# Optimization experiments

Hardware: AMD Instinct MI355X
Metric: run time of the kernel (lower is better)

The kernel has to match this reference:

```python
import jax, jax.numpy as jnp
from jax import lax
import numpy as np

ATTN = 32  # attn_size window
PAD, SOS = 1, 2


def setup_inputs() -> dict:
    key = jax.random.key(0)
    ks = jax.random.split(key, 20)
    B, L, V, E, H = 16, 64, 32000, 512, 512
    sc = 0.02
    inp = {
        "s_tensor": jax.random.randint(ks[0], (B, L), 0, V, dtype=jnp.int32),
        "parents_tensor": jax.random.randint(ks[1], (L,), 0, L, dtype=jnp.int32),
        "emb": jax.random.normal(ks[2], (V, E), jnp.float32) * sc,
        "W_hid": jax.random.normal(ks[3], (H, H), jnp.float32) * sc,
        "b_hid": jnp.zeros((H,), jnp.float32),
        "v_w": jax.random.normal(ks[4], (H,), jnp.float32) * sc,
        "v_b": jnp.zeros((1,), jnp.float32),
        "W_ctx": jax.random.normal(ks[5], (E + H, H), jnp.float32) * sc,
        "b_ctx": jnp.zeros((H,), jnp.float32),
        "W_ih": jax.random.normal(ks[6], (H, 4 * H), jnp.float32) * sc,
        "W_hh": jax.random.normal(ks[7], (H, 4 * H), jnp.float32) * sc,
        "b_lstm": jnp.zeros((4 * H,), jnp.float32),
        "W_glob": jax.random.normal(ks[8], (3 * H, V), jnp.float32) * sc,
        "b_glob": jnp.zeros((V,), jnp.float32),
        "w_sw": jax.random.normal(ks[9], (2 * H,), jnp.float32) * sc,
        "b_sw": jnp.zeros((1,), jnp.float32),
    }
    return inp


def _decode(emb, W_hid, b_hid, v_w, v_b, W_ctx, b_ctx, W_ih, W_hh, b_lstm,
            W_glob, b_glob, w_sw, b_sw, s_tensor, parents_tensor):
    B, L = s_tensor.shape
    H = W_hid.shape[0]
    A = ATTN
    # teacher forcing: input at step t is SOS for t=0, else s_tensor[:, t-1]
    inputs = jnp.concatenate(
        [jnp.full((B, 1), SOS, s_tensor.dtype), s_tensor[:, : L - 2]], axis=1)  # [B, L-1]
    targets = s_tensor[:, 1:]  # [B, L-1]
    hs_buf0 = jnp.zeros((B, A + L, H), jnp.float32)  # past decoder hidden states (A zero-pad prefix)
    h0 = jnp.zeros((B, H), jnp.float32)
    c0 = jnp.zeros((B, H), jnp.float32)

    def step(carry, xs):
        h, c, hs_buf = carry
        tok, tgt, par, t = xs
        x = emb[tok]  # [B, E]
        # memory = last A decoder hidden states (steps t-A .. t-1)
        mem = lax.dynamic_slice(hs_buf, (0, t, 0), (B, A, H))
        # Bahdanau-style scores: v^T tanh(W_hidden(h) + mem), masked to valid window
        q = h @ W_hid + b_hid  # [B, H]
        scores = jnp.tanh(q[:, None, :] + mem) @ v_w + v_b  # [B, A]
        valid = jnp.arange(A) >= (A - t)
        scores = jnp.where(valid[None, :], scores, -1e20)
        attn = jax.nn.softmax(scores, axis=1)
        context = jnp.einsum('ba,bah->bh', attn, mem)
        hid = jax.nn.selu(jnp.concatenate([x, context], axis=1) @ W_ctx + b_ctx)
        # single-step LSTM cell (PyTorch gate order i,f,g,o)
        gates = hid @ W_ih + h @ W_hh + b_lstm
        i, f, g, o = jnp.split(gates, 4, axis=1)
        c_new = jax.nn.sigmoid(f) * c + jax.nn.sigmoid(i) * jnp.tanh(g)
        h_new = jax.nn.sigmoid(o) * jnp.tanh(c_new)
        # parent hidden state
        p = jnp.clip(par, 0, jnp.maximum(t - 1, 0))
        h_par = lax.dynamic_slice(hs_buf, (0, A + p, 0), (B, 1, H))[:, 0]
        logits = jnp.concatenate([h_new, c_new, h_par], axis=1) @ W_glob + b_glob
        logp = jax.nn.log_softmax(logits, axis=1)
        s = jax.nn.sigmoid(jnp.concatenate([h_new, c_new], axis=1) @ w_sw + b_sw)  # [B,1]
        out = s[:, None] * logp if s.ndim == 1 else s * logp  # pointer switch on global dist
        nll = -jnp.take_along_axis(out, tgt[:, None].astype(jnp.int32), axis=1)[:, 0]
        nll = jnp.where(tgt != PAD, nll, 0.0)
        pred = jnp.argmax(out, axis=1).astype(jnp.int32)
        hs_buf = lax.dynamic_update_slice(hs_buf, h_new[:, None, :], (0, A + t, 0))
        return (h_new, c_new, hs_buf), (nll, pred)

    T = L - 1
    xs = (inputs.T, targets.T, parents_tensor[:T], jnp.arange(T, dtype=jnp.int32))
    _, (nlls, preds) = lax.scan(step, (h0, c0, hs_buf0), xs)
    loss = nlls.sum() / B
    return loss, preds.T  # [B, L-1] predicted tokens


def reference(s_tensor, parents_tensor, emb, W_hid, b_hid, v_w, v_b, W_ctx, b_ctx,
              W_ih, W_hh, b_lstm, W_glob, b_glob, w_sw, b_sw):
    return _decode(emb, W_hid, b_hid, v_w, v_b, W_ctx, b_ctx, W_ih, W_hh, b_lstm,
                   W_glob, b_glob, w_sw, b_sw, s_tensor, parents_tensor)
```

## Files before the change

kernel.cpp:

```cpp
#include <hip/hip_runtime.h>
#include <math.h>

#define BB 16
#define LL 64
#define TT 63
#define HH 512
#define AA 32
#define VV 32000
#define NCHUNK 250
#define CHW 128
#define TGRP 3
#define NTG 21
#define PAD_TOK 1
#define SOS_TOK 2
#define HSROW 96
#define ZK 1536
#define FLTMAX 3.402823466e38f

__device__ __forceinline__ float sigm(float x){ return 1.0f/(1.0f + __expf(-x)); }

__global__ __launch_bounds__(256) void k_pre(const int* __restrict__ s, const float* __restrict__ emb,
                      const float* __restrict__ Wctx, const float* __restrict__ bctx,
                      float* __restrict__ xwpre)
{
    int t = blockIdx.x >> 3;
    int jc = blockIdx.x & 7;
    int tid = threadIdx.x;
    int jj = tid & 63, bq = tid >> 6;
    int j = jc*64 + jj;
    __shared__ int toks[BB];
    __shared__ float xs[BB][HH];
    if (tid < BB) {
        int b = tid;
        toks[b] = (t == 0) ? SOS_TOK : s[b*LL + (t-1)];
    }
    __syncthreads();
    for (int i = tid; i < BB*HH; i += 256) {
        int b = i >> 9, k = i & 511;
        xs[b][k] = emb[(size_t)toks[b]*HH + k];
    }
    __syncthreads();
    float acc[4];
    #pragma unroll
    for (int u = 0; u < 4; u++) acc[u] = bctx[j];
    for (int k = 0; k < HH; k += 4) {
        float w0 = Wctx[(k+0)*HH+j], w1 = Wctx[(k+1)*HH+j],
              w2 = Wctx[(k+2)*HH+j], w3 = Wctx[(k+3)*HH+j];
        #pragma unroll
        for (int u = 0; u < 4; u++) {
            int b = bq*4 + u;
            float4 hv = *reinterpret_cast<const float4*>(&xs[b][k]);
            acc[u] = fmaf(hv.x, w0, acc[u]);
            acc[u] = fmaf(hv.y, w1, acc[u]);
            acc[u] = fmaf(hv.z, w2, acc[u]);
            acc[u] = fmaf(hv.w, w3, acc[u]);
        }
    }
    #pragma unroll
    for (int u = 0; u < 4; u++) {
        int b = bq*4 + u;
        xwpre[((size_t)t*BB + b)*HH + j] = acc[u];
    }
}

__global__ __launch_bounds__(256) void k_tw(const float* __restrict__ Wg, float4* __restrict__ Wt4b)
{
    int kg = blockIdx.x / 125;
    int cb = blockIdx.x % 125;
    int col = cb*256 + threadIdx.x;
    const float* w0 = Wg + (size_t)(4*kg)*VV + col;
    float4 v;
    v.x = w0[0];
    v.y = w0[VV];
    v.z = w0[2*VV];
    v.w = w0[3*VV];
    Wt4b[(size_t)(col >> 6)*(384*64) + kg*64 + (col & 63)] = v;
}

__global__ __launch_bounds__(256) void k_twl(const float* __restrict__ W, float4* __restrict__ WT)
{
    int kg = blockIdx.x >> 3;
    int cb = blockIdx.x & 7;
    int col = cb*256 + threadIdx.x;
    const float* w0 = W + (size_t)(4*kg)*2048 + col;
    float4 v;
    v.x = w0[0];
    v.y = w0[2048];
    v.z = w0[2*2048];
    v.w = w0[3*2048];
    WT[(size_t)kg*2048 + col] = v;
}

__device__ void finish_step(int tp, int b, int tid,
                            const int* __restrict__ s,
                            const float* __restrict__ lb,
                            const float* __restrict__ pmax,
                            const float* __restrict__ spart,
                            const float* __restrict__ bsw,
                            float* __restrict__ nll, float* __restrict__ out,
                            float* cv, int* ci, double* sdd, float* extra)
{
    float v = -FLTMAX;
    if (tid < NCHUNK) v = pmax[tid*BB + b];
    cv[tid] = v; __syncthreads();
    for (int sft = 256; sft >= 1; sft >>= 1) {
        if (tid < sft) cv[tid] = fmaxf(cv[tid], cv[tid+sft]);
        __syncthreads();
    }
    float gmax = cv[0];
    __syncthreads();

    const float* Lb = lb + (size_t)b*VV;
    double sd = 0.0;
    for (int col = tid; col < VV; col += 512) {
        float d1 = Lb[col] - gmax;
        double u = (double)d1, e;
        if (u < -0.25) {
            e = exp(u);
        } else {
            e = 1.0 + u*(1.0/7.0);
            e = 1.0 + u*e*(1.0/6.0);
            e = 1.0 + u*e*(1.0/5.0);
            e = 1.0 + u*e*(1.0/4.0);
            e = 1.0 + u*e*(1.0/3.0);
            e = 1.0 + u*e*(1.0/2.0);
            e = 1.0 + u*e;
        }
        sd += e;
    }
    sdd[tid] = sd; __syncthreads();
    for (int sft = 256; sft >= 1; sft >>= 1) {
        if (tid < sft) sdd[tid] += sdd[tid+sft];
        __syncthreads();
    }
    float logS = logf((float)sdd[0]);

    float z = bsw[0];
    #pragma unroll
    for (int i2 = 0; i2 < 8; i2++) z += spart[b*8 + i2];
    float sF = 1.0f/(1.0f + expf(-z));
    __syncthreads();

    int tg = s[b*LL + tp + 1];
    float best = -FLTMAX; int bidx = 0x7fffffff;
    for (int col = tid; col < VV; col += 512) {
        float d1 = Lb[col] - gmax;
        float d2 = d1 - logS;
        float pq = sF * d2;
        if (pq > best) { best = pq; bidx = col; }
        if (col == tg) extra[0] = pq;
    }
    cv[tid] = best; ci[tid] = bidx; __syncthreads();
    for (int sft = 256; sft >= 1; sft >>= 1) {
        if (tid < sft) {
            float v2 = cv[tid+sft]; int i2 = ci[tid+sft];
            if (v2 > cv[tid] || (v2 == cv[tid] && i2 < ci[tid])) { cv[tid] = v2; ci[tid] = i2; }
        }
        __syncthreads();
    }
    if (tid == 0) {
        out[1 + b*TT + tp] = (float)ci[0];
        nll[tp*BB + b] = (tg != PAD_TOK) ? -extra[0] : 0.f;
    }
    __syncthreads();
}

__global__ __launch_bounds__(512) void k_fin_all(
    int t0, const int* __restrict__ s,
    const float* __restrict__ lbBase, unsigned long long lbStride,
    const float* __restrict__ pmaxBase, unsigned long long pmaxStride,
    const float* __restrict__ spartAll, const float* __restrict__ bsw,
    float* __restrict__ nll, float* __restrict__ out)
{
    __shared__ float cv[512];
    __shared__ int   ci[512];
    __shared__ double sdd[512];
    __shared__ float extra[2];
    int idx = blockIdx.x >> 4;
    int tp = t0 + idx, b = blockIdx.x & 15;
    finish_step(tp, b, threadIdx.x, s,
                lbBase + (size_t)idx * lbStride,
                pmaxBase + (size_t)idx * pmaxStride,
                spartAll + (size_t)tp * 128,
                bsw, nll, out, cv, ci, sdd, extra);
}

__global__ __launch_bounds__(512) void k_attn(
    int t,
    const float* __restrict__ Whid, const float* __restrict__ bhid,
    const float* __restrict__ vw, const float* __restrict__ vb,
    const float* __restrict__ Wctx, const float* __restrict__ xwpre,
    const float* __restrict__ hs, float* __restrict__ hidg)
{
    int b = blockIdx.x, tid = threadIdx.x;
    __shared__ float hsh[HH], qs[HH], ctxs[HH];
    __shared__ float sc[AA], at[AA];
    const float* hp = hs + ((size_t)b*HSROW + (AA + t - 1))*HH;
    hsh[tid] = hp[tid];
    __syncthreads();
    {
        int j = tid;
        float acc = bhid[j];
        for (int k = 0; k < HH; k += 4) {
            float4 hv = *reinterpret_cast<const float4*>(&hsh[k]);
            acc = fmaf(hv.x, Whid[(k+0)*HH+j], acc);
            acc = fmaf(hv.y, Whid[(k+1)*HH+j], acc);
            acc = fmaf(hv.z, Whid[(k+2)*HH+j], acc);
            acc = fmaf(hv.w, Whid[(k+3)*HH+j], acc);
        }
        qs[j] = acc;
    }
    __syncthreads();
    {
        int w = tid >> 6, lane = tid & 63;
        for (int r = 0; r < 4; r++) {
            int a = w + 8*r;
            const float* mem = hs + ((size_t)b*HSROW + (t + a))*HH;
            float p = 0.f;
            for (int j = lane; j < HH; j += 64) p += tanhf(qs[j] + mem[j]) * vw[j];
            for (int m = 32; m >= 1; m >>= 1) p += __shfl_xor(p, m);
            if (lane == 0) sc[a] = (a >= AA - t) ? (p + vb[0]) : -1e20f;
        }
    }
    __syncthreads();
    if (tid < 64) {
        float v = (tid < 32) ? sc[tid] : -FLTMAX;
        float m = v;
        for (int sh = 16; sh >= 1; sh >>= 1) m = fmaxf(m, __shfl_xor(m, sh));
        float e = (tid < 32) ? __expf(v - m) : 0.f;
        float ss = e;
        for (int sh = 16; sh >= 1; sh >>= 1) ss += __shfl_xor(ss, sh);
        if (tid < 32) at[tid] = e / ss;
    }
    __syncthreads();
    {
        int j = tid;
        float ctx = 0.f;
        for (int a = 0; a < AA; a++)
            ctx += at[a] * hs[((size_t)b*HSROW + (t + a))*HH + j];
        ctxs[j] = ctx;
    }
    __syncthreads();
    {
        int j = tid;
        float acc = xwpre[((size_t)t*BB + b)*HH + j];
        const float* W2 = Wctx + (size_t)HH*HH;
        for (int k = 0; k < HH; k += 4) {
            float4 hv = *reinterpret_cast<const float4*>(&ctxs[k]);
            acc = fmaf(hv.x, W2[(k+0)*HH+j], acc);
            acc = fmaf(hv.y, W2[(k+1)*HH+j], acc);
            acc = fmaf(hv.z, W2[(k+2)*HH+j], acc);
            acc = fmaf(hv.w, W2[(k+3)*HH+j], acc);
        }
        const float scl = 1.0507009873554805f, al = 1.6732632423543772f;
        hidg[b*HH + j] = (acc > 0.f) ? scl*acc : scl*al*expm1f(acc);
    }
}

__global__ __launch_bounds__(256) void k_gates(
    int t, const int* __restrict__ parents,
    const float4* __restrict__ WihT, const float4* __restrict__ WhhT,
    const float* __restrict__ blstm, const float* __restrict__ wsw,
    const float* __restrict__ hidg, float* __restrict__ hs,
    float* __restrict__ cvec, float* __restrict__ spart,
    float* __restrict__ zbuf)
{
    int bid = blockIdx.x, b = bid >> 3, hc = bid & 7, h0 = hc*64;
    int tid = threadIdx.x, g = tid >> 6, jj = tid & 63, j = h0 + jj, col = g*HH + j;
    __shared__ float hid_s[HH], h_s[HH];
    __shared__ float gsl[4][64];
    const float* hp = hs + ((size_t)b*HSROW + (AA + t - 1))*HH;
    for (int k = tid; k < HH; k += 256) { hid_s[k] = hidg[b*HH + k]; h_s[k] = hp[k]; }
    __syncthreads();
    float acc = blstm[col];
    #pragma unroll 8
    for (int kg = 0; kg < 128; kg++) {
        float4 w = WihT[(size_t)kg*2048 + col];
        float4 hv = *reinterpret_cast<const float4*>(&hid_s[kg*4]);
        acc = fmaf(hv.x, w.x, acc);
        acc = fmaf(hv.y, w.y, acc);
        acc = fmaf(hv.z, w.z, acc);
        acc = fmaf(hv.w, w.w, acc);
    }
    #pragma unroll 8
    for (int kg = 0; kg < 128; kg++) {
        float4 w = WhhT[(size_t)kg*2048 + col];
        float4 hv = *reinterpret_cast<const float4*>(&h_s[kg*4]);
        acc = fmaf(hv.x, w.x, acc);
        acc = fmaf(hv.y, w.y, acc);
        acc = fmaf(hv.z, w.z, acc);
        acc = fmaf(hv.w, w.w, acc);
    }
    gsl[g][jj] = acc;
    __syncthreads();
    if (tid >= 64 && tid < 128) {
        int jj2 = tid - 64;
        int par = parents[t];
        int tm1 = (t - 1 > 0) ? (t - 1) : 0;
        int p = (par < 0) ? 0 : ((par > tm1) ? tm1 : par);
        float v = (t == 0) ? 0.f : hs[((size_t)b*HSROW + (AA + p))*HH + h0 + jj2];
        zbuf[(size_t)b*ZK + 2*HH + h0 + jj2] = v;
    }
    if (tid < 64) {
        float gi = gsl[0][jj], gf = gsl[1][jj], gg = gsl[2][jj], go = gsl[3][jj];
        float cp = cvec[b*HH + j];
        float cn = sigm(gf)*cp + sigm(gi)*tanhf(gg);
        float hn = sigm(go)*tanhf(cn);
        cvec[b*HH + j] = cn;
        hs[((size_t)b*HSROW + (AA + t))*HH + j] = hn;
        zbuf[(size_t)b*ZK + j] = hn;
        zbuf[(size_t)b*ZK + HH + j] = cn;
        float sp = hn*wsw[j] + cn*wsw[HH + j];
        for (int m = 32; m >= 1; m >>= 1) sp += __shfl_xor(sp, m);
        if (jj == 0) spart[b*8 + hc] = sp;
    }
}

template<int NT>
__device__ __forceinline__ void logits_body4(int chunk, int base_t,
    const float4* __restrict__ Wt4b, const float* __restrict__ bg,
    const float* __restrict__ zBase, size_t zStride,
    float* __restrict__ lbBase, size_t lbStride,
    float* __restrict__ pmaxBase, size_t pmaxStride,
    float* zs)
{
    int tid = threadIdx.x;
    int lane = tid & 63;
    int cg = lane & 31;
    int kh = lane >> 5;
    int b0 = (tid >> 6) * 4;

    const float4* wt0 = Wt4b + (size_t)(chunk*2 + 0)*(384*64) + cg;
    const float4* wt1 = Wt4b + (size_t)(chunk*2 + 0)*(384*64) + cg + 32;
    const float4* wt2 = Wt4b + (size_t)(chunk*2 + 1)*(384*64) + cg;
    const float4* wt3 = Wt4b + (size_t)(chunk*2 + 1)*(384*64) + cg + 32;

    float acc[NT][4][4];
    #pragma unroll
    for (int tt = 0; tt < NT; tt++)
        #pragma unroll
        for (int cc = 0; cc < 4; cc++) {
            float binit = (kh == 0) ? bg[chunk*CHW + cg + 32*cc] : 0.f;
            #pragma unroll
            for (int u = 0; u < 4; u++) acc[tt][cc][u] = binit;
        }

    const int NF4 = NT*16*2*16;
    for (int kc = 0; kc < 3; kc++) {
        for (int sub = 0; sub < 4; sub++) {
            __syncthreads();
            for (int p = 0; p < NF4/256; p++) {
                int fi = tid + p*256;
                int kl4 = fi & 15;
                int khs = (fi >> 4) & 1;
                int u   = (fi >> 5) & 15;
                int tt  = fi >> 9;
                const float* src = zBase + (size_t)(base_t + tt)*zStride + kc*512
                                 + (size_t)u*ZK + khs*256 + sub*64 + kl4*4;
                *reinterpret_cast<float4*>(&zs[(((tt*16 + u)*2 + khs)*64) + kl4*4]) =
                    *reinterpret_cast<const float4*>(src);
            }
            __syncthreads();
            int kgb = kc*128 + kh*64 + sub*16;
            const float4* w0P = wt0 + (size_t)kgb*64;
            const float4* w1P = wt1 + (size_t)kgb*64;
            const float4* w2P = wt2 + (size_t)kgb*64;
            const float4* w3P = wt3 + (size_t)kgb*64;
            #pragma unroll 4
            for (int kl = 0; kl < 16; kl++) {
                float4 w0 = w0P[kl*64];
                float4 w1 = w1P[kl*64];
                float4 w2 = w2P[kl*64];
                float4 w3 = w3P[kl*64];
                #pragma unroll
                for (int tt = 0; tt < NT; tt++) {
                    #pragma unroll
                    for (int u = 0; u < 4; u++) {
                        float4 z = *reinterpret_cast<const float4*>(
                            &zs[(((tt*16 + (b0 + u))*2 + kh)*64) + kl*4]);
                        acc[tt][0][u] = fmaf(z.x, w0.x, fmaf(z.y, w0.y, fmaf(z.z, w0.z, fmaf(z.w, w0.w, acc[tt][0][u]))));
                        acc[tt][1][u] = fmaf(z.x, w1.x, fmaf(z.y, w1.y, fmaf(z.z, w1.z, fmaf(z.w, w1.w, acc[tt][1][u]))));
                        acc[tt][2][u] = fmaf(z.x, w2.x, fmaf(z.y, w2.y, fmaf(z.z, w2.z, fmaf(z.w, w2.w, acc[tt][2][u]))));
                        acc[tt][3][u] = fmaf(z.x, w3.x, fmaf(z.y, w3.y, fmaf(z.z, w3.z, fmaf(z.w, w3.w, acc[tt][3][u]))));
                    }
                }
            }
        }
    }

    #pragma unroll
    for (int tt = 0; tt < NT; tt++) {
        float* lb   = lbBase   + (size_t)(base_t + tt)*lbStride;
        float* pmax = pmaxBase + (size_t)(base_t + tt)*pmaxStride;
        #pragma unroll
        for (int u = 0; u < 4; u++) {
            float vmax = -FLTMAX;
            #pragma unroll
            for (int cc = 0; cc < 4; cc++) {
                float a = acc[tt][cc][u];
                float oth = __shfl_xor(a, 32);
                float tot = a + oth;
                if (kh == 0) lb[(size_t)(b0 + u)*VV + chunk*CHW + cg + 32*cc] = tot;
                vmax = fmaxf(vmax, tot);
            }
            for (int m = 16; m >= 1; m >>= 1) vmax = fmaxf(vmax, __shfl_xor(vmax, m));
            if (lane == 0) pmax[chunk*BB + b0 + u] = vmax;
        }
    }
}

__global__ __launch_bounds__(256) void k_logits_mega3(
    const float4* __restrict__ Wt4b, const float* __restrict__ bg,
    const float* __restrict__ zBase,
    float* __restrict__ lbBase, float* __restrict__ pmaxBase)
{
    __shared__ float zs[TGRP*16*2*64];
    logits_body4<TGRP>(blockIdx.y, blockIdx.x * TGRP, Wt4b, bg,
                       zBase, (size_t)BB*ZK, lbBase, 512000, pmaxBase, 4000, zs);
}

__global__ __launch_bounds__(256) void k_logits_T1(
    const float4* __restrict__ Wt4b, const float* __restrict__ bg,
    const float* __restrict__ zbuf,
    float* __restrict__ lb, float* __restrict__ pmax)
{
    __shared__ float zs[1*16*2*64];
    logits_body4<1>(blockIdx.x, 0, Wt4b, bg, zbuf, 0, lb, 0, pmax, 0, zs);
}

__global__ __launch_bounds__(256) void k_logits_F(
    const float* __restrict__ Wg, const float* __restrict__ bg,
    const float* __restrict__ zbuf,
    float* __restrict__ lb, float* __restrict__ pmax)
{
    int tid = threadIdx.x;
    int chunk = blockIdx.x;
    int lane = tid & 63;
    int cg = lane & 31;
    int kh = lane >> 5;
    int b0 = (tid >> 6) * 4;

    float acc[4][4];
    #pragma unroll
    for (int cc = 0; cc < 4; cc++) {
        float binit = (kh == 0) ? bg[chunk*CHW + cg + 32*cc] : 0.f;
        #pragma unroll
        for (int u = 0; u < 4; u++) acc[cc][u] = binit;
    }

    for (int kc = 0; kc < 3; kc++) {
        const float* zb = zbuf + kc*512 + (size_t)b0*ZK;
        #pragma unroll 2
        for (int k4 = 0; k4 < 64; k4++) {
            int kb = kh*256 + k4*4;
            const float* wr = Wg + (size_t)(kc*512 + kb)*VV + chunk*CHW + cg;
            float4 w[4];
            #pragma unroll
            for (int cc = 0; cc < 4; cc++) {
                w[cc].x = wr[32*cc];
                w[cc].y = wr[(size_t)VV + 32*cc];
                w[cc].z = wr[(size_t)2*VV + 32*cc];
                w[cc].w = wr[(size_t)3*VV + 32*cc];
            }
            #pragma unroll
            for (int u = 0; u < 4; u++) {
                float4 z = *reinterpret_cast<const float4*>(&zb[(size_t)u*ZK + kb]);
                #pragma unroll
                for (int cc = 0; cc < 4; cc++)
                    acc[cc][u] = fmaf(z.x, w[cc].x, fmaf(z.y, w[cc].y, fmaf(z.z, w[cc].z, fmaf(z.w, w[cc].w, acc[cc][u]))));
            }
        }
    }

    #pragma unroll
    for (int u = 0; u < 4; u++) {
        float vmax = -FLTMAX;
        #pragma unroll
        for (int cc = 0; cc < 4; cc++) {
            float a = acc[cc][u];
            float oth = __shfl_xor(a, 32);
            float tot = a + oth;
            if (kh == 0) lb[(size_t)(b0 + u)*VV + chunk*CHW + cg + 32*cc] = tot;
            vmax = fmaxf(vmax, tot);
        }
        for (int m = 16; m >= 1; m >>= 1) vmax = fmaxf(vmax, __shfl_xor(vmax, m));
        if (lane == 0) pmax[chunk*BB + b0 + u] = vmax;
    }
}

__global__ __launch_bounds__(256) void k_final_loss(
    const float* __restrict__ nll, float* __restrict__ out)
{
    __shared__ double cs2[256];
    int tid = threadIdx.x;
    double psm = 0.0;
    for (int i = tid; i < TT*BB; i += 256) psm += (double)nll[i];
    cs2[tid] = psm; __syncthreads();
    for (int sft = 128; sft >= 1; sft >>= 1) {
        if (tid < sft) cs2[tid] += cs2[tid+sft];
        __syncthreads();
    }
    if (tid == 0) out[0] = (float)(cs2[0] / (double)BB);
}

extern "C" void kernel_launch(void* const* d_in, const int* in_sizes, int n_in,
                              void* d_out, int out_size, void* d_ws, size_t ws_size,
                              hipStream_t stream)
{
    const int*   s_tok = (const int*)  d_in[0];
    const int*   par   = (const int*)  d_in[1];
    const float* emb   = (const float*)d_in[2];
    const float* Whid  = (const float*)d_in[3];
    const float* bhid  = (const float*)d_in[4];
    const float* vw    = (const float*)d_in[5];
    const float* vb    = (const float*)d_in[6];
    const float* Wctx  = (const float*)d_in[7];
    const float* bctx  = (const float*)d_in[8];
    const float* Wih   = (const float*)d_in[9];
    const float* Whh   = (const float*)d_in[10];
    const float* blstm = (const float*)d_in[11];
    const float* Wg    = (const float*)d_in[12];
    const float* bg    = (const float*)d_in[13];
    const float* wsw   = (const float*)d_in[14];
    const float* bsw   = (const float*)d_in[15];
    float* out = (float*)d_out;

    size_t ws_f = ws_size / sizeof(float);
    const size_t base_f = 786432 + 8192 + 516096 + 8192;
    const size_t com_f  = 8064 + 1008 + 2*1048576;
    const size_t full_f = base_f + com_f + (size_t)63*4000 + (size_t)63*512000
                        + (size_t)63*24576 + 49152000;
    const size_t mid_f  = base_f + com_f + 4000 + 512000 + 24576 + 49152000;
    int mode = (ws_f >= full_f) ? 2 : ((ws_f >= mid_f) ? 1 : 0);

    float* ws = (float*)d_ws;
    size_t off = 0;
    float* hs      = ws + off; off += 786432;
    float* cvec    = ws + off; off += 8192;
    float* xwpre   = ws + off; off += 516096;
    float* hidg    = ws + off; off += 8192;
    float* pmaxAll = ws + off; off += (mode == 2) ? (size_t)63*4000 : 4000;
    float* spartAll= ws + off; off += 8064;
    float* nll     = ws + off; off += 1008;
    float* zbufAll = ws + off; off += (mode == 2) ? (size_t)63*24576 : 24576;
    float* lbAll   = ws + off; off += (mode == 2) ? (size_t)63*512000 : 512000;
    float4* WihT   = (float4*)(ws + off); off += 1048576;
    float4* WhhT   = (float4*)(ws + off); off += 1048576;
    float4* Wt4b   = (float4*)(ws + off);

    hipMemsetAsync(hs, 0, (786432 + 8192) * sizeof(float), stream);

    hipLaunchKernelGGL(k_twl, dim3(1024), dim3(256), 0, stream, Wih, WihT);
    hipLaunchKernelGGL(k_twl, dim3(1024), dim3(256), 0, stream, Whh, WhhT);
    if (mode >= 1) {
        hipLaunchKernelGGL(k_tw, dim3(384*125), dim3(256), 0, stream, Wg, Wt4b);
    }
    hipLaunchKernelGGL(k_pre, dim3(TT*8), dim3(256), 0, stream, s_tok, emb, Wctx, bctx, xwpre);

    if (mode == 2) {
        for (int t = 0; t < TT; t++) {
            hipLaunchKernelGGL(k_attn, dim3(BB), dim3(512), 0, stream,
                t, Whid, bhid, vw, vb, Wctx, xwpre, hs, hidg);
            hipLaunchKernelGGL(k_gates, dim3(128), dim3(256), 0, stream,
                t, par, WihT, WhhT, blstm, wsw, hidg, hs, cvec,
                spartAll + (size_t)t*128, zbufAll + (size_t)t*BB*ZK);
        }
        hipLaunchKernelGGL(k_logits_mega3, dim3(NTG, NCHUNK), dim3(256), 0, stream,
            Wt4b, bg, zbufAll, lbAll, pmaxAll);
        hipLaunchKernelGGL(k_fin_all, dim3(TT*BB), dim3(512), 0, stream,
            0, s_tok, lbAll, (unsigned long long)512000,
            pmaxAll, (unsigned long long)4000,
            spartAll, bsw, nll, out);
    } else {
        for (int t = 0; t < TT; t++) {
            hipLaunchKernelGGL(k_attn, dim3(BB), dim3(512), 0, stream,
                t, Whid, bhid, vw, vb, Wctx, xwpre, hs, hidg);
            hipLaunchKernelGGL(k_gates, dim3(128), dim3(256), 0, stream,
                t, par, WihT, WhhT, blstm, wsw, hidg, hs, cvec,
                spartAll + (size_t)t*128, zbufAll);
            if (mode >= 1) {
                hipLaunchKernelGGL(k_logits_T1, dim3(NCHUNK), dim3(256), 0, stream,
                    Wt4b, bg, zbufAll, lbAll, pmaxAll);
            } else {
                hipLaunchKernelGGL(k_logits_F, dim3(NCHUNK), dim3(256), 0, stream,
                    Wg, bg, zbufAll, lbAll, pmaxAll);
            }
            hipLaunchKernelGGL(k_fin_all, dim3(BB), dim3(512), 0, stream,
                t, s_tok, lbAll, (unsigned long long)0, pmaxAll, (unsigned long long)0,
                spartAll, bsw, nll, out);
        }
    }
    hipLaunchKernelGGL(k_final_loss, dim3(1), dim3(256), 0, stream, nll, out);
}
```

Before: 4.797 ms.

## Prefetch z tiles into registers, remap logits grid for XCD locality, nontemporal stores

The logits mega-kernel now loads the next z sub-tile from global memory into registers while the current tile is consumed, which hides global latency behind the FMA loop. The 2D grid is flattened and remapped so consecutive blocks on the same XCD (round-robin by 8) share a W_glob chunk. Logit stores use nontemporal hints so they bypass cache pollution. In exchange it uses more registers for the prefetch buffer, and 8*672 blocks exceed the real work, so some blocks exit early.

New measurement: 5.118 ms. 1.07x slower.

```diff
diff --git a/kernel.cpp b/kernel.cpp
--- a/kernel.cpp
+++ b/kernel.cpp
@@ -345,22 +345,37 @@
             for (int u = 0; u < 4; u++) acc[tt][cc][u] = binit;
         }
 
-    const int NF4 = NT*16*2*16;
+    constexpr int NP = NT*2;
+    float4 pre[NP];
+    #define PD(p) int fi##p = tid + (p)*256; \
+                  int kl4##p = fi##p & 15; int khs##p = (fi##p >> 4) & 1; \
+                  int uu##p = (fi##p >> 5) & 15; int tt##p = fi##p >> 9;
+    auto LD = [&](int kc, int sub) {
+        #pragma unroll
+        for (int p = 0; p < NP; p++) {
+            int fi = tid + p*256;
+            int kl4 = fi & 15, khs = (fi >> 4) & 1, uu = (fi >> 5) & 15, tt = fi >> 9;
+            const float* src = zBase + (size_t)(base_t + tt)*zStride + kc*512
+                             + (size_t)uu*ZK + khs*256 + sub*64 + kl4*4;
+            pre[p] = *reinterpret_cast<const float4*>(src);
+        }
+    };
+    LD(0, 0);
     for (int kc = 0; kc < 3; kc++) {
         for (int sub = 0; sub < 4; sub++) {
             __syncthreads();
-            for (int p = 0; p < NF4/256; p++) {
+            #pragma unroll
+            for (int p = 0; p < NP; p++) {
                 int fi = tid + p*256;
-                int kl4 = fi & 15;
-                int khs = (fi >> 4) & 1;
-                int u   = (fi >> 5) & 15;
-                int tt  = fi >> 9;
-                const float* src = zBase + (size_t)(base_t + tt)*zStride + kc*512
-                                 + (size_t)u*ZK + khs*256 + sub*64 + kl4*4;
-                *reinterpret_cast<float4*>(&zs[(((tt*16 + u)*2 + khs)*64) + kl4*4]) =
-                    *reinterpret_cast<const float4*>(src);
+                int kl4 = fi & 15, khs = (fi >> 4) & 1, uu = (fi >> 5) & 15, tt = fi >> 9;
+                *reinterpret_cast<float4*>(&zs[(((tt*16 + uu)*2 + khs)*64) + kl4*4]) = pre[p];
             }
             __syncthreads();
+            {
+                int nsub = sub + 1, nkc = kc;
+                if (nsub == 4) { nsub = 0; nkc++; }
+                if (nkc < 3) LD(nkc, nsub);
+            }
             int kgb = kc*128 + kh*64 + sub*16;
             const float4* w0P = wt0 + (size_t)kgb*64;
             const float4* w1P = wt1 + (size_t)kgb*64;
@@ -400,7 +415,8 @@
                 float a = acc[tt][cc][u];
                 float oth = __shfl_xor(a, 32);
                 float tot = a + oth;
-                if (kh == 0) lb[(size_t)(b0 + u)*VV + chunk*CHW + cg + 32*cc] = tot;
+                if (kh == 0)
+                    __builtin_nontemporal_store(tot, &lb[(size_t)(b0 + u)*VV + chunk*CHW + cg + 32*cc]);
                 vmax = fmaxf(vmax, tot);
             }
             for (int m = 16; m >= 1; m >>= 1) vmax = fmaxf(vmax, __shfl_xor(vmax, m));
@@ -415,7 +431,13 @@
     float* __restrict__ lbBase, float* __restrict__ pmaxBase)
 {
     __shared__ float zs[TGRP*16*2*64];
-    logits_body4<TGRP>(blockIdx.y, blockIdx.x * TGRP, Wt4b, bg,
+    int h = blockIdx.x;
+    int r = h & 7, m = h >> 3;
+    int w = r*672 + m;
+    if (w >= NTG*NCHUNK) return;
+    int chunk = w / NTG;
+    int base_t = (w % NTG) * TGRP;
+    logits_body4<TGRP>(chunk, base_t, Wt4b, bg,
                        zBase, (size_t)BB*ZK, lbBase, 512000, pmaxBase, 4000, zs);
 }
 
@@ -565,7 +587,7 @@
                 t, par, WihT, WhhT, blstm, wsw, hidg, hs, cvec,
                 spartAll + (size_t)t*128, zbufAll + (size_t)t*BB*ZK);
         }
-        hipLaunchKernelGGL(k_logits_mega3, dim3(NTG, NCHUNK), dim3(256), 0, stream,
+        hipLaunchKernelGGL(k_logits_mega3, dim3(8*672), dim3(256), 0, stream,
             Wt4b, bg, zbufAll, lbAll, pmaxAll);
         hipLaunchKernelGGL(k_fin_all, dim3(TT*BB), dim3(512), 0, stream,
             0, s_tok, lbAll, (unsigned long long)512000,
```
